# Kernel tuning notes

Hardware: AMD Instinct MI355X
Metric: run time of the kernel (lower is better)

Reference implementation:

```python
import jax, jax.numpy as jnp
import numpy as np

B, LH, HF = 65536, 128, 32
VC_MIN = 0.0


def _theta_init():
    # Deterministic parameter init, matching the torch constructor defaults.
    def spinv(x):
        return float(np.log(np.exp(max(x, 1e-4)) - 1.0 + 1e-6))
    vals = [
        0.0,                                  # alpha_raw: log(0.5/(1-0.5))
        float(np.log(np.exp(1.0) - 1.0 + 1e-6)),   # c_raw  (c_init=1.0)
        float(np.log(np.exp(0.1) - 1.0 + 1e-6)),   # kappa_raw (kappa_init=0.1)
        float(np.log(np.exp(0.15) - 1.0 + 1e-6)),  # vc_raw (vc_eff=0.15)
        -6.0,   # log_qx
        -6.0,   # log_qu
        -5.0,   # log_r
        0.0,    # log_q_scale
        -6.0,   # log_p0_xx
        -4.0,   # log_p0_uu
        spinv(0.1),   # a1_raw
        spinv(0.05),  # d1_raw
        spinv(0.5),   # d2_raw
        spinv(0.5),   # d3_raw
        0.0,    # b1
        0.0,    # b2
        0.1,    # beta
        float(np.arctanh(0.9)),  # rho_m_raw
        -4.0,   # log_qm
        -4.0,   # log_p0_mm
    ]
    return np.asarray(vals, dtype=np.float32)


def setup_inputs() -> dict:
    key = jax.random.key(0)
    k1, k2, k3, k4, k5 = jax.random.split(key, 5)
    return {
        "v_hist": jax.random.normal(k1, (B, LH), dtype=jnp.float32),
        "dt_hist": 0.01 + 0.1 * jax.random.uniform(k2, (B, LH), dtype=jnp.float32),
        "x_obs_hist": jax.random.normal(k3, (B, LH), dtype=jnp.float32),
        "v_fut": jax.random.normal(k4, (B, HF), dtype=jnp.float32),
        "dt_fut": 0.01 + 0.1 * jax.random.uniform(k5, (B, HF), dtype=jnp.float32),
        "theta": jnp.asarray(_theta_init()),
    }


def _forward(v_hist, dt_hist, x_obs_hist, v_fut, dt_fut, theta):
    sp = jax.nn.softplus
    alpha = jax.nn.sigmoid(theta[0])
    c = sp(theta[1]); kappa = sp(theta[2]); vc = sp(theta[3]) + VC_MIN
    qx = jnp.exp(theta[4]); qu = jnp.exp(theta[5]); R = jnp.exp(theta[6])
    qs = jnp.exp(theta[7]); p0xx = jnp.exp(theta[8]); p0uu = jnp.exp(theta[9])
    a1 = sp(theta[10]); d1 = sp(theta[11]); d2 = sp(theta[12]); d3 = sp(theta[13])
    b1 = theta[14]; b2 = theta[15]; beta = theta[16]
    rho_m = jnp.tanh(theta[17]); qm = jnp.exp(theta[18]); p0mm = jnp.exp(theta[19])

    Bn, Lh = v_hist.shape
    dtype = v_hist.dtype
    eye = jnp.eye(3, dtype=dtype)

    def predict(s, P, v, dv, dt):
        x, u, m = s[:, 0], s[:, 1], s[:, 2]
        rho = jnp.exp(-alpha * dt)
        forcing = jax.nn.relu(v * v - vc * vc)
        cl = (-a1 * u + b1 * v + b2 * dv
              - d1 * u * u - d2 * u * jnp.abs(v) - d3 * u * jnp.abs(u))
        x_p = x + u * dt
        u_p = rho * u - kappa * x * dt + c * forcing * dt + cl * dt + beta * m
        m_p = rho_m * m
        s_p = jnp.stack([x_p, u_p, m_p], axis=1)
        z = jnp.zeros_like(dt); o = jnp.ones_like(dt)
        Fm = jnp.stack([
            jnp.stack([o, dt, z], axis=1),
            jnp.stack([-kappa * dt, rho, beta * o], axis=1),
            jnp.stack([z, z, rho_m * o], axis=1)], axis=1)  # [B,3,3]
        qdiag = jnp.stack([qs * qx * dt, qs * qu * dt, qm * o], axis=1)  # [B,3]
        P_p = jnp.einsum('bij,bjk,blk->bil', Fm, P, Fm) + qdiag[:, :, None] * eye
        return s_p, P_p

    def update(s, P, y):
        innov = y - s[:, 0]
        S = P[:, 0, 0] + R
        K = P[:, :, 0] / S[:, None]            # [B,3]
        s_u = s + K * innov[:, None]
        IKH = eye - K[:, :, None] * eye[0]     # I - K H, H = [1,0,0]
        P_u = (jnp.einsum('bij,bjk,blk->bil', IKH, P, IKH)
               + R * (K[:, :, None] * K[:, None, :]))
        return s_u, P_u

    s0 = jnp.zeros((Bn, 3), dtype).at[:, 0].set(x_obs_hist[:, 0])
    P0 = jnp.broadcast_to(jnp.diag(jnp.stack([p0xx, p0uu, p0mm])).astype(dtype),
                          (Bn, 3, 3))

    # History steps k = 1 .. Lh-1 (scan over time axis, [T, B] layout)
    v_h = v_hist[:, :Lh - 1].T
    dv_h = jnp.concatenate(
        [jnp.zeros((1, Bn), dtype), (v_hist[:, 1:Lh - 1] - v_hist[:, :Lh - 2]).T], axis=0)
    dt_h = jnp.maximum(dt_hist[:, 1:], 1e-6).T
    y_h = x_obs_hist[:, 1:].T

    def hist_step(carry, inp):
        s, P = carry
        v, dv, dt, y = inp
        s, P = predict(s, P, v, dv, dt)
        s, P = update(s, P, y)
        return (s, P), None

    (s, P), _ = jax.lax.scan(hist_step, (s0, P0), (v_h, dv_h, dt_h, y_h))

    # Future rollout (predict only)
    v_f = v_fut.T
    dv_f = (v_fut - jnp.concatenate([v_hist[:, -1:], v_fut[:, :-1]], axis=1)).T
    dt_f = jnp.maximum(dt_fut, 1e-6).T

    def fut_step(carry, inp):
        s, P = carry
        v, dv, dt = inp
        s, P = predict(s, P, v, dv, dt)
        return (s, P), (s[:, 0], P[:, 0, 0], s[:, 1])

    _, (x_preds, x_vars, u_ests) = jax.lax.scan(fut_step, (s, P), (v_f, dv_f, dt_f))
    return x_preds.T, x_vars.T, u_ests.T  # each [B, Hf]


def reference(v_hist, dt_hist, x_obs_hist, v_fut, dt_fut, theta):
    return _forward(v_hist, dt_hist, x_obs_hist, v_fut, dt_fut, theta)
```

## Files before the change

kernel.cpp:

```cpp
#include <hip/hip_runtime.h>
#include <math.h>

#define BATCH 65536
#define LHIST 128
#define HFUT  32
#define CH    16

__device__ __forceinline__ float softplusf(float x) {
    return fmaxf(x, 0.0f) + log1pf(expf(-fabsf(x)));
}

__global__ __launch_bounds__(256, 1) void kalman_fwd(
    const float* __restrict__ v_hist,
    const float* __restrict__ dt_hist,
    const float* __restrict__ x_obs,
    const float* __restrict__ v_fut,
    const float* __restrict__ dt_fut,
    const float* __restrict__ theta,
    float* __restrict__ out)
{
    const int b = blockIdx.x * blockDim.x + threadIdx.x;

    const float alpha = 1.0f / (1.0f + expf(-theta[0]));
    const float c     = softplusf(theta[1]);
    const float kappa = softplusf(theta[2]);
    const float vc    = softplusf(theta[3]);
    const float qx    = expf(theta[4]);
    const float qu    = expf(theta[5]);
    const float Rn    = expf(theta[6]);
    const float qs    = expf(theta[7]);
    const float p0xx  = expf(theta[8]);
    const float p0uu  = expf(theta[9]);
    const float a1    = softplusf(theta[10]);
    const float d1    = softplusf(theta[11]);
    const float d2    = softplusf(theta[12]);
    const float d3    = softplusf(theta[13]);
    const float b1    = theta[14];
    const float b2    = theta[15];
    const float beta  = theta[16];
    const float rho_m = tanhf(theta[17]);
    const float qm    = expf(theta[18]);
    const float p0mm  = expf(theta[19]);
    const float vc2   = vc * vc;
    const float qxs   = qs * qx;
    const float qus   = qs * qu;
    const float nal2e = -alpha * 1.44269504088896340736f;

    float sx = 0.0f, su = 0.0f, sm = 0.0f;
    float p00 = p0xx, p01 = 0.0f, p02 = 0.0f, p11 = p0uu, p12 = 0.0f, p22 = p0mm;

    auto predict = [&](float v, float dv, float dt_raw) {
        float dt  = fmaxf(dt_raw, 1e-6f);
        float rho = __builtin_amdgcn_exp2f(nal2e * dt);
        float forcing = fmaxf(v * v - vc2, 0.0f);
        float cl = -a1 * su + b1 * v + b2 * dv
                 - d1 * su * su - d2 * su * fabsf(v) - d3 * su * fabsf(su);
        float kdt = kappa * dt;
        float x_p = sx + su * dt;
        float u_p = rho * su - kdt * sx + c * forcing * dt + cl * dt + beta * sm;
        float m_p = rho_m * sm;
        float f0 = p00 + dt * p01;
        float f1 = p01 + dt * p11;
        float f2 = p02 + dt * p12;
        float g0 = -kdt * p00 + rho * p01 + beta * p02;
        float g1 = -kdt * p01 + rho * p11 + beta * p12;
        float g2 = -kdt * p02 + rho * p12 + beta * p22;
        float n00 = f0 + dt * f1 + qxs * dt;
        float n01 = -kdt * f0 + rho * f1 + beta * f2;
        float n02 = rho_m * f2;
        float n11 = -kdt * g0 + rho * g1 + beta * g2 + qus * dt;
        float n12 = rho_m * g2;
        float n22 = rho_m * rho_m * p22 + qm;
        sx = x_p; su = u_p; sm = m_p;
        p00 = n00; p01 = n01; p02 = n02; p11 = n11; p12 = n12; p22 = n22;
    };

    auto update = [&](float y) {
        float innov = y - sx;
        float S    = p00 + Rn;
        float Sinv = __builtin_amdgcn_rcpf(S);
        float K0 = p00 * Sinv, K1 = p01 * Sinv, K2 = p02 * Sinv;
        sx += K0 * innov; su += K1 * innov; sm += K2 * innov;
        float a = 1.0f - K0;
        float n00 = a * a * p00 + Rn * K0 * K0;
        float n01 = a * (p01 - K1 * p00) + Rn * K0 * K1;
        float n02 = a * (p02 - K2 * p00) + Rn * K0 * K2;
        float n11 = S * K1 * K1 - 2.0f * K1 * p01 + p11;
        float n12 = S * K1 * K2 - K2 * p01 - K1 * p02 + p12;
        float n22 = S * K2 * K2 - 2.0f * K2 * p02 + p22;
        p00 = n00; p01 = n01; p02 = n02; p11 = n11; p12 = n12; p22 = n22;
    };

    const float4* v4  = (const float4*)(v_hist  + (size_t)b * LHIST);
    const float4* d4  = (const float4*)(dt_hist + (size_t)b * LHIST);
    const float4* y4  = (const float4*)(x_obs   + (size_t)b * LHIST);

    float cv[CH], cd[CH], cy[CH];
    float nv[CH], nd[CH], ny[CH];

    auto load_chunk = [&](float (&vv)[CH], float (&dd)[CH], float (&yy)[CH], int k) {
        float4* V = (float4*)vv; float4* D = (float4*)dd; float4* Y = (float4*)yy;
        #pragma unroll
        for (int i = 0; i < CH / 4; ++i) {
            V[i] = v4[(CH / 4) * k + i];
            D[i] = d4[(CH / 4) * k + i];
            Y[i] = y4[(CH / 4) * k + i];
        }
    };

    load_chunk(cv, cd, cy, 0);
    load_chunk(nv, nd, ny, 1);

    sx = cy[0];
    predict(cv[0], 0.0f, cd[1]); update(cy[1]);
    #pragma unroll
    for (int i = 1; i < CH - 1; ++i) {
        predict(cv[i], cv[i] - cv[i - 1], cd[i + 1]); update(cy[i + 1]);
    }
    float v_bridge  = cv[CH - 1];
    float dv_bridge = cv[CH - 1] - cv[CH - 2];

    #pragma unroll 1
    for (int k = 1; k < LHIST / CH; ++k) {
        #pragma unroll
        for (int i = 0; i < CH; ++i) { cv[i] = nv[i]; cd[i] = nd[i]; cy[i] = ny[i]; }
        if (k < LHIST / CH - 1) load_chunk(nv, nd, ny, k + 1);
        predict(v_bridge, dv_bridge, cd[0]); update(cy[0]);
        predict(cv[0], cv[0] - v_bridge, cd[1]); update(cy[1]);
        #pragma unroll
        for (int i = 1; i < CH - 1; ++i) {
            predict(cv[i], cv[i] - cv[i - 1], cd[i + 1]); update(cy[i + 1]);
        }
        v_bridge  = cv[CH - 1];
        dv_bridge = cv[CH - 1] - cv[CH - 2];
    }

    const float4* vf4 = (const float4*)(v_fut  + (size_t)b * HFUT);
    const float4* df4 = (const float4*)(dt_fut + (size_t)b * HFUT);
    float vf[HFUT], df[HFUT];
    {
        float4* VF = (float4*)vf; float4* DF = (float4*)df;
        #pragma unroll
        for (int i = 0; i < HFUT / 4; ++i) { VF[i] = vf4[i]; DF[i] = df4[i]; }
    }

    float oxp[HFUT], oxv[HFUT], oue[HFUT];
    float vp = v_bridge;
    #pragma unroll
    for (int j = 0; j < HFUT; ++j) {
        predict(vf[j], vf[j] - vp, df[j]);
        vp = vf[j];
        oxp[j] = sx; oxv[j] = p00; oue[j] = su;
    }

    float4* xp = (float4*)(out + (size_t)b * HFUT);
    float4* xv = (float4*)(out + (size_t)BATCH * HFUT + (size_t)b * HFUT);
    float4* ue = (float4*)(out + 2 * (size_t)BATCH * HFUT + (size_t)b * HFUT);
    float4* OXP = (float4*)oxp; float4* OXV = (float4*)oxv; float4* OUE = (float4*)oue;
    #pragma unroll
    for (int i = 0; i < HFUT / 4; ++i) {
        xp[i] = OXP[i]; xv[i] = OXV[i]; ue[i] = OUE[i];
    }
}

extern "C" void kernel_launch(void* const* d_in, const int* in_sizes, int n_in,
                              void* d_out, int out_size, void* d_ws, size_t ws_size,
                              hipStream_t stream) {
    const float* v_hist  = (const float*)d_in[0];
    const float* dt_hist = (const float*)d_in[1];
    const float* x_obs   = (const float*)d_in[2];
    const float* v_fut   = (const float*)d_in[3];
    const float* dt_fut  = (const float*)d_in[4];
    const float* theta   = (const float*)d_in[5];
    float* out = (float*)d_out;

    dim3 grid(BATCH / 256), block(256);
    hipLaunchKernelGGL(kalman_fwd, grid, block, 0, stream,
                       v_hist, dt_hist, x_obs, v_fut, dt_fut, theta, out);
}
```

Measured before the change: 164.2 us.

## Shrink register chunks to float4 groups and stream future outputs per group

Replaces the 16-element double-buffered register chunks with single float4 groups prefetched one step ahead for the history scan. The future rollout now loads inputs and writes outputs per float4 group instead of staging all 32 steps in register arrays. The aim is to cut VGPR pressure so more waves can be resident and hide memory latency. The cost is smaller load batches and less distance to hide each load, plus extra loop overhead from unroll 1. It also hoists rho_m squared into a constant.

After: 200.7 us. 1.22x slower.

```diff
diff --git a/kernel.cpp b/kernel.cpp
--- a/kernel.cpp
+++ b/kernel.cpp
@@ -4,7 +4,6 @@
 #define BATCH 65536
 #define LHIST 128
 #define HFUT  32
-#define CH    16
 
 __device__ __forceinline__ float softplusf(float x) {
     return fmaxf(x, 0.0f) + log1pf(expf(-fabsf(x)));
@@ -44,6 +43,7 @@
     const float vc2   = vc * vc;
     const float qxs   = qs * qx;
     const float qus   = qs * qu;
+    const float rm2   = rho_m * rho_m;
     const float nal2e = -alpha * 1.44269504088896340736f;
 
     float sx = 0.0f, su = 0.0f, sm = 0.0f;
@@ -70,7 +70,7 @@
         float n02 = rho_m * f2;
         float n11 = -kdt * g0 + rho * g1 + beta * g2 + qus * dt;
         float n12 = rho_m * g2;
-        float n22 = rho_m * rho_m * p22 + qm;
+        float n22 = rm2 * p22 + qm;
         sx = x_p; su = u_p; sm = m_p;
         p00 = n00; p01 = n01; p02 = n02; p11 = n11; p12 = n12; p22 = n22;
     };
@@ -91,75 +91,70 @@
         p00 = n00; p01 = n01; p02 = n02; p11 = n11; p12 = n12; p22 = n22;
     };
 
-    const float4* v4  = (const float4*)(v_hist  + (size_t)b * LHIST);
-    const float4* d4  = (const float4*)(dt_hist + (size_t)b * LHIST);
-    const float4* y4  = (const float4*)(x_obs   + (size_t)b * LHIST);
+    const float4* v4 = (const float4*)(v_hist  + (size_t)b * LHIST);
+    const float4* d4 = (const float4*)(dt_hist + (size_t)b * LHIST);
+    const float4* y4 = (const float4*)(x_obs   + (size_t)b * LHIST);
 
-    float cv[CH], cd[CH], cy[CH];
-    float nv[CH], nd[CH], ny[CH];
+    float vp1, vp2;
 
-    auto load_chunk = [&](float (&vv)[CH], float (&dd)[CH], float (&yy)[CH], int k) {
-        float4* V = (float4*)vv; float4* D = (float4*)dd; float4* Y = (float4*)yy;
+    float4 cvv = v4[0], cdd = d4[0], cyy = y4[0];
+    float4 pv  = v4[1], pd  = d4[1], py  = y4[1];
+    {
+        const float* vv = (const float*)&cvv;
+        const float* dd = (const float*)&cdd;
+        const float* yy = (const float*)&cyy;
+        sx = yy[0]; vp1 = vv[0]; vp2 = vv[0];
         #pragma unroll
-        for (int i = 0; i < CH / 4; ++i) {
-            V[i] = v4[(CH / 4) * k + i];
-            D[i] = d4[(CH / 4) * k + i];
-            Y[i] = y4[(CH / 4) * k + i];
+        for (int m = 1; m < 4; ++m) {
+            float vcur = vv[m];
+            predict(vp1, vp1 - vp2, dd[m]);
+            update(yy[m]);
+            vp2 = vp1; vp1 = vcur;
         }
-    };
-
-    load_chunk(cv, cd, cy, 0);
-    load_chunk(nv, nd, ny, 1);
-
-    sx = cy[0];
-    predict(cv[0], 0.0f, cd[1]); update(cy[1]);
-    #pragma unroll
-    for (int i = 1; i < CH - 1; ++i) {
-        predict(cv[i], cv[i] - cv[i - 1], cd[i + 1]); update(cy[i + 1]);
     }
-    float v_bridge  = cv[CH - 1];
-    float dv_bridge = cv[CH - 1] - cv[CH - 2];
 
     #pragma unroll 1
-    for (int k = 1; k < LHIST / CH; ++k) {
+    for (int g = 1; g < LHIST / 4; ++g) {
+        cvv = pv; cdd = pd; cyy = py;
+        int gn = (g < LHIST / 4 - 1) ? g + 1 : g;
+        pv = v4[gn]; pd = d4[gn]; py = y4[gn];
+        const float* vv = (const float*)&cvv;
+        const float* dd = (const float*)&cdd;
+        const float* yy = (const float*)&cyy;
         #pragma unroll
-        for (int i = 0; i < CH; ++i) { cv[i] = nv[i]; cd[i] = nd[i]; cy[i] = ny[i]; }
-        if (k < LHIST / CH - 1) load_chunk(nv, nd, ny, k + 1);
-        predict(v_bridge, dv_bridge, cd[0]); update(cy[0]);
-        predict(cv[0], cv[0] - v_bridge, cd[1]); update(cy[1]);
-        #pragma unroll
-        for (int i = 1; i < CH - 1; ++i) {
-            predict(cv[i], cv[i] - cv[i - 1], cd[i + 1]); update(cy[i + 1]);
+        for (int m = 0; m < 4; ++m) {
+            float vcur = vv[m];
+            predict(vp1, vp1 - vp2, dd[m]);
+            update(yy[m]);
+            vp2 = vp1; vp1 = vcur;
         }
-        v_bridge  = cv[CH - 1];
-        dv_bridge = cv[CH - 1] - cv[CH - 2];
     }
 
     const float4* vf4 = (const float4*)(v_fut  + (size_t)b * HFUT);
     const float4* df4 = (const float4*)(dt_fut + (size_t)b * HFUT);
-    float vf[HFUT], df[HFUT];
-    {
-        float4* VF = (float4*)vf; float4* DF = (float4*)df;
-        #pragma unroll
-        for (int i = 0; i < HFUT / 4; ++i) { VF[i] = vf4[i]; DF[i] = df4[i]; }
-    }
-
-    float oxp[HFUT], oxv[HFUT], oue[HFUT];
-    float vp = v_bridge;
-    #pragma unroll
-    for (int j = 0; j < HFUT; ++j) {
-        predict(vf[j], vf[j] - vp, df[j]);
-        vp = vf[j];
-        oxp[j] = sx; oxv[j] = p00; oue[j] = su;
-    }
-
     float4* xp = (float4*)(out + (size_t)b * HFUT);
     float4* xv = (float4*)(out + (size_t)BATCH * HFUT + (size_t)b * HFUT);
     float4* ue = (float4*)(out + 2 * (size_t)BATCH * HFUT + (size_t)b * HFUT);
-    float4* OXP = (float4*)oxp; float4* OXV = (float4*)oxv; float4* OUE = (float4*)oue;
-    #pragma unroll
-    for (int i = 0; i < HFUT / 4; ++i) {
-        xp[i] = OXP[i]; xv[i] = OXV[i]; ue[i] = OUE[i];
+
+    float vp = vp1;
+    float4 fv = vf4[0], fd = df4[0];
+    float4 qv = vf4[1], qd = df4[1];
+    #pragma unroll 1
+    for (int g = 0; g < HFUT / 4; ++g) {
+        const float* vv = (const float*)&fv;
+        const float* dd = (const float*)&fd;
+        float4 ox, ov, ou;
+        float* oxp = (float*)&ox; float* ovp = (float*)&ov; float* oup = (float*)&ou;
+        #pragma unroll
+        for (int m = 0; m < 4; ++m) {
+            predict(vv[m], vv[m] - vp, dd[m]);
+            vp = vv[m];
+            oxp[m] = sx; ovp[m] = p00; oup[m] = su;
+        }
+        xp[g] = ox; xv[g] = ov; ue[g] = ou;
+        fv = qv; fd = qd;
+        int gn = (g < HFUT / 4 - 2) ? g + 2 : HFUT / 4 - 1;
+        qv = vf4[gn]; qd = df4[gn];
     }
 }
 
```
